# Performance work log

Measured on AMD Instinct MI355X. Metric: run time of the kernel, lower is better.

## Reference

```python
import jax, jax.numpy as jnp
import numpy as np

TEMPERATURE = 0.07
N_BANK = 1_000_000
DIM = 128
BATCH = 1024
K_NEIGH = 200


def _prob_density(memory_bank, v, idx):
    # memory_bank: [N, D], v: [B, D] (L2-normalized), idx: [B, K]
    vals = memory_bank[idx]                      # [B, K, D] gather
    dots = jnp.einsum('bkd,bd->bk', vals, v)     # per-item dot products
    return jnp.sum(jnp.exp(dots / TEMPERATURE), axis=1)  # [B]


def setup_inputs() -> dict:
    key = jax.random.key(0)
    k1, k2, k3, k4 = jax.random.split(key, 4)
    codes = jax.random.normal(k1, (BATCH, DIM), dtype=jnp.float32)
    memory_bank = jax.random.normal(k2, (N_BANK, DIM), dtype=jnp.float32)
    # memory bank rows are unit-normalized in the LA setup
    memory_bank = memory_bank / jnp.linalg.norm(memory_bank, axis=1, keepdims=True)
    idx_background = jax.random.randint(k3, (BATCH, K_NEIGH), 0, N_BANK, dtype=jnp.int64)
    idx_close = jax.random.randint(k4, (BATCH, K_NEIGH), 0, N_BANK, dtype=jnp.int64)
    return {
        'codes': codes,
        'memory_bank': memory_bank,
        'idx_background': idx_background,
        'idx_close': idx_close,
    }


def reference(codes, memory_bank, idx_background, idx_close):
    # v = F.normalize(codes, p=2, dim=1)
    v = codes / jnp.linalg.norm(codes, axis=1, keepdims=True)
    d1 = _prob_density(memory_bank, v, idx_background)
    d2 = _prob_density(memory_bank, v, idx_close)
    # loss_cluster = log(d1) - log(d2)
    return jnp.log(d1) - jnp.log(d2)
```

## Files before the change

kernel.cpp:

```cpp
#include <hip/hip_runtime.h>
#include <math.h>


constexpr int DIM = 128;
constexpr int KN  = 200;
constexpr int RPG = 25;
constexpr int UF  = 5;
constexpr float INV_T = 1.0f / 0.07f;

__global__ __launch_bounds__(256, 4)
void lal_kernel(const float* __restrict__ codes,
                const float* __restrict__ bank,
                const int*   __restrict__ idx_bg,
                const int*   __restrict__ idx_cl,
                float*       __restrict__ out)
{
    const int b   = blockIdx.x;
    const int tid = threadIdx.x;

    __shared__ float v[DIM];
    __shared__ int   s_ib[KN];
    __shared__ int   s_ic[KN];
    __shared__ float wsum[4];
    __shared__ float red1[8];
    __shared__ float red2[8];
    __shared__ float s_rnorm;

    if (tid < KN) {
        s_ib[tid] = idx_bg[b * KN + tid];
        s_ic[tid] = idx_cl[b * KN + tid];
    }

    float c  = (tid < DIM) ? codes[b * DIM + tid] : 0.0f;
    float ss = c * c;
    #pragma unroll
    for (int m = 32; m > 0; m >>= 1) ss += __shfl_xor(ss, m, 64);
    if ((tid & 63) == 0) wsum[tid >> 6] = ss;
    __syncthreads();
    if (tid == 0) {
        float t = wsum[0] + wsum[1] + wsum[2] + wsum[3];
        s_rnorm = 1.0f / sqrtf(t);
    }
    __syncthreads();
    if (tid < DIM) v[tid] = c * s_rnorm;
    __syncthreads();

    const int group = tid >> 5;
    const int lane  = tid & 31;

    const float4 vv = ((const float4*)v)[lane];
    const int kbase = group * RPG;

    float sum1 = 0.0f, sum2 = 0.0f;

    #pragma unroll 1
    for (int j = 0; j < RPG; j += UF) {
        float4 x1[UF], x2[UF];
        #pragma unroll
        for (int u = 0; u < UF; ++u) {
            const int r1 = s_ib[kbase + j + u];
            const int r2 = s_ic[kbase + j + u];
            x1[u] = ((const float4*)(bank + (size_t)r1 * DIM))[lane];
            x2[u] = ((const float4*)(bank + (size_t)r2 * DIM))[lane];
        }
        #pragma unroll
        for (int u = 0; u < UF; ++u) {
            float d1 = x1[u].x * vv.x + x1[u].y * vv.y + x1[u].z * vv.z + x1[u].w * vv.w;
            float d2 = x2[u].x * vv.x + x2[u].y * vv.y + x2[u].z * vv.z + x2[u].w * vv.w;
            #pragma unroll
            for (int m = 16; m > 0; m >>= 1) {
                d1 += __shfl_xor(d1, m, 64);
                d2 += __shfl_xor(d2, m, 64);
            }
            sum1 += __expf(d1 * INV_T);
            sum2 += __expf(d2 * INV_T);
        }
    }

    if (lane == 0) { red1[group] = sum1; red2[group] = sum2; }
    __syncthreads();
    if (tid == 0) {
        float D1 = 0.0f, D2 = 0.0f;
        #pragma unroll
        for (int g = 0; g < 8; ++g) { D1 += red1[g]; D2 += red2[g]; }
        out[b] = logf(D1) - logf(D2);
    }
}

extern "C" void kernel_launch(void* const* d_in, const int* in_sizes, int n_in,
                              void* d_out, int out_size, void* d_ws, size_t ws_size,
                              hipStream_t stream)
{
    const float* codes  = (const float*)d_in[0];
    const float* bank   = (const float*)d_in[1];
    const int*   idx_bg = (const int*)d_in[2];
    const int*   idx_cl = (const int*)d_in[3];
    float*       out    = (float*)d_out;

    const int batch = in_sizes[0] / DIM;
    lal_kernel<<<batch, 256, 0, stream>>>(codes, bank, idx_bg, idx_cl, out);
}
```

Measured before the change: 587.2 us.

## Stream gathered bank rows into LDS with triple-buffered async global_load_lds

```diff
diff --git a/kernel.cpp b/kernel.cpp
--- a/kernel.cpp
+++ b/kernel.cpp
@@ -2,34 +2,39 @@
 #include <math.h>
 
 
-constexpr int DIM = 128;
-constexpr int KN  = 200;
-constexpr int RPG = 25;
-constexpr int UF  = 5;
+constexpr int DIM   = 128;
+constexpr int KN    = 200;
+constexpr int HALF  = 100;
+constexpr int TROWS = 4;
+constexpr int NT    = HALF / TROWS;
 constexpr float INV_T = 1.0f / 0.07f;
 
-__global__ __launch_bounds__(256, 4)
+typedef const __attribute__((address_space(1))) void gvoid_t;
+typedef __attribute__((address_space(3))) void lvoid_t;
+
+__global__ __launch_bounds__(256, 6)
 void lal_kernel(const float* __restrict__ codes,
                 const float* __restrict__ bank,
                 const int*   __restrict__ idx_bg,
                 const int*   __restrict__ idx_cl,
                 float*       __restrict__ out)
 {
-    const int b   = blockIdx.x;
-    const int tid = threadIdx.x;
+    const int b    = blockIdx.x;
+    const int tid  = threadIdx.x;
+    const int w    = tid >> 6;
+    const int lane = tid & 63;
 
-    __shared__ float v[DIM];
-    __shared__ int   s_ib[KN];
-    __shared__ int   s_ic[KN];
+    __shared__ alignas(16) float v[DIM];
+    __shared__ int   s_idx[4 * HALF];
+    __shared__ alignas(16) float tiles[4][3][TROWS * DIM];
     __shared__ float wsum[4];
-    __shared__ float red1[8];
-    __shared__ float red2[8];
+    __shared__ float red[4];
     __shared__ float s_rnorm;
 
-    if (tid < KN) {
-        s_ib[tid] = idx_bg[b * KN + tid];
-        s_ic[tid] = idx_cl[b * KN + tid];
-    }
+    const int* ip    = (w < 2) ? idx_bg : idx_cl;
+    const int  kbase = (w & 1) * HALF;
+    for (int k = lane; k < HALF; k += 64)
+        s_idx[w * HALF + k] = ip[b * KN + kbase + k];
 
     float c  = (tid < DIM) ? codes[b * DIM + tid] : 0.0f;
     float ss = c * c;
@@ -45,46 +50,63 @@
     if (tid < DIM) v[tid] = c * s_rnorm;
     __syncthreads();
 
-    const int group = tid >> 5;
-    const int lane  = tid & 31;
+    const int s = lane & 15;
+    const int r = lane >> 4;
+    const float4 vv0 = ((const float4*)v)[s];
+    const float4 vv1 = ((const float4*)v)[s + 16];
 
-    const float4 vv = ((const float4*)v)[lane];
-    const int kbase = group * RPG;
+    const float* bank_lane = bank + (lane & 31) * 4;
+    const int*   midx = &s_idx[w * HALF];
+    float* const tb   = &tiles[w][0][0];
+    float sum = 0.0f;
 
-    float sum1 = 0.0f, sum2 = 0.0f;
+    auto STAGE = [&](int t, int bsel) {
+        int r0 = midx[4 * t     + (lane >> 5)];
+        int r1 = midx[4 * t + 2 + (lane >> 5)];
+        const float* g0 = bank_lane + (size_t)r0 * DIM;
+        const float* g1 = bank_lane + (size_t)r1 * DIM;
+        float* d0 = tb + bsel * (TROWS * DIM);
+        float* d1 = d0 + 2 * DIM;
+        __builtin_amdgcn_global_load_lds((gvoid_t*)g0, (lvoid_t*)d0, 16, 0, 0);
+        __builtin_amdgcn_global_load_lds((gvoid_t*)g1, (lvoid_t*)d1, 16, 0, 0);
+    };
 
-    #pragma unroll 1
-    for (int j = 0; j < RPG; j += UF) {
-        float4 x1[UF], x2[UF];
-        #pragma unroll
-        for (int u = 0; u < UF; ++u) {
-            const int r1 = s_ib[kbase + j + u];
-            const int r2 = s_ic[kbase + j + u];
-            x1[u] = ((const float4*)(bank + (size_t)r1 * DIM))[lane];
-            x2[u] = ((const float4*)(bank + (size_t)r2 * DIM))[lane];
-        }
-        #pragma unroll
-        for (int u = 0; u < UF; ++u) {
-            float d1 = x1[u].x * vv.x + x1[u].y * vv.y + x1[u].z * vv.z + x1[u].w * vv.w;
-            float d2 = x2[u].x * vv.x + x2[u].y * vv.y + x2[u].z * vv.z + x2[u].w * vv.w;
-            #pragma unroll
-            for (int m = 16; m > 0; m >>= 1) {
-                d1 += __shfl_xor(d1, m, 64);
-                d2 += __shfl_xor(d2, m, 64);
-            }
-            sum1 += __expf(d1 * INV_T);
-            sum2 += __expf(d2 * INV_T);
-        }
+    auto COMPUTE = [&](int bsel) {
+        const float4* T = (const float4*)(tb + bsel * (TROWS * DIM));
+        float4 x0 = T[r * 32 + s];
+        float4 x1 = T[r * 32 + s + 16];
+        float d = x0.x * vv0.x + x0.y * vv0.y + x0.z * vv0.z + x0.w * vv0.w
+                + x1.x * vv1.x + x1.y * vv1.y + x1.z * vv1.z + x1.w * vv1.w;
+        d += __shfl_xor(d, 1, 16);
+        d += __shfl_xor(d, 2, 16);
+        d += __shfl_xor(d, 4, 16);
+        d += __shfl_xor(d, 8, 16);
+        float e = __expf(d * INV_T);
+        if (s == 0) sum += e;
+    };
+
+    STAGE(0, 0);
+    STAGE(1, 1);
+    int bsel = 0;
+    for (int t = 0; t < NT - 2; ++t) {
+        STAGE(t + 2, (bsel + 2) % 3);
+        asm volatile("s_waitcnt vmcnt(4)" ::: "memory");
+        COMPUTE(bsel);
+        __builtin_amdgcn_sched_barrier(0);
+        bsel = (bsel + 1) % 3;
     }
+    asm volatile("s_waitcnt vmcnt(2)" ::: "memory");
+    COMPUTE(bsel);
+    bsel = (bsel + 1) % 3;
+    asm volatile("s_waitcnt vmcnt(0)" ::: "memory");
+    COMPUTE(bsel);
 
-    if (lane == 0) { red1[group] = sum1; red2[group] = sum2; }
+    #pragma unroll
+    for (int m = 32; m > 0; m >>= 1) sum += __shfl_xor(sum, m, 64);
+    if (lane == 0) red[w] = sum;
     __syncthreads();
-    if (tid == 0) {
-        float D1 = 0.0f, D2 = 0.0f;
-        #pragma unroll
-        for (int g = 0; g < 8; ++g) { D1 += red1[g]; D2 += red2[g]; }
-        out[b] = logf(D1) - logf(D2);
-    }
+    if (tid == 0)
+        out[b] = logf(red[0] + red[1]) - logf(red[2] + red[3]);
 }
 
 extern "C" void kernel_launch(void* const* d_in, const int* in_sizes, int n_in,
```

After: 590.6 us. Within noise of the previous version (+0.6%).

## Split gather into per-list blocks with full unroll and separate finalize kernel

Applied to the files above, without the earlier changes.

```diff
diff --git a/kernel.cpp b/kernel.cpp
--- a/kernel.cpp
+++ b/kernel.cpp
@@ -2,18 +2,96 @@
 #include <math.h>
 
 
-constexpr int DIM = 128;
-constexpr int KN  = 200;
-constexpr int RPG = 25;
-constexpr int UF  = 5;
+constexpr int   DIM   = 128;
+constexpr int   KN    = 200;
+constexpr int   RPG   = 25;
 constexpr float INV_T = 1.0f / 0.07f;
 
+
+__global__ __launch_bounds__(256, 3)
+void k_gather(const float* __restrict__ codes,
+              const float* __restrict__ bank,
+              const int*   __restrict__ idx_bg,
+              const int*   __restrict__ idx_cl,
+              float*       __restrict__ dacc,
+              int batch)
+{
+    const int bid  = blockIdx.x;
+    const int b    = bid >> 1;
+    const int list = bid & 1;
+    const int tid  = threadIdx.x;
+
+    const int* __restrict__ ip = list ? idx_cl : idx_bg;
+
+    __shared__ alignas(16) float v[DIM];
+    __shared__ int   s_idx[KN];
+    __shared__ float wsum[4];
+    __shared__ float red[8];
+    __shared__ float s_rnorm;
+
+    if (tid < KN) s_idx[tid] = ip[b * KN + tid];
+
+    float c  = (tid < DIM) ? codes[b * DIM + tid] : 0.0f;
+    float ss = c * c;
+    #pragma unroll
+    for (int m = 32; m > 0; m >>= 1) ss += __shfl_xor(ss, m, 64);
+    if ((tid & 63) == 0) wsum[tid >> 6] = ss;
+    __syncthreads();
+    if (tid == 0) {
+        float t = wsum[0] + wsum[1] + wsum[2] + wsum[3];
+        s_rnorm = 1.0f / sqrtf(t);
+    }
+    __syncthreads();
+    if (tid < DIM) v[tid] = c * s_rnorm;
+    __syncthreads();
+
+    const int group = tid >> 5;
+    const int lane  = tid & 31;
+    const float4 vv = ((const float4*)v)[lane];
+    const int kbase = group * RPG;
+
+    float4 x[RPG];
+    #pragma unroll
+    for (int u = 0; u < RPG; ++u) {
+        const int r = s_idx[kbase + u];
+        x[u] = ((const float4*)(bank + (size_t)r * DIM))[lane];
+    }
+
+    float sum = 0.0f;
+    #pragma unroll
+    for (int u = 0; u < RPG; ++u) {
+        float d = x[u].x * vv.x + x[u].y * vv.y + x[u].z * vv.z + x[u].w * vv.w;
+        #pragma unroll
+        for (int m = 16; m > 0; m >>= 1) d += __shfl_xor(d, m, 64);
+        sum += __expf(d * INV_T);
+    }
+
+    if (lane == 0) red[group] = sum;
+    __syncthreads();
+    if (tid == 0) {
+        float D = 0.0f;
+        #pragma unroll
+        for (int g = 0; g < 8; ++g) D += red[g];
+        dacc[list * batch + b] = D;
+    }
+}
+
+__global__ __launch_bounds__(256)
+void k_fin(const float* __restrict__ dacc, float* __restrict__ out, int batch)
+{
+    const int b = blockIdx.x * blockDim.x + threadIdx.x;
+    if (b < batch) out[b] = logf(dacc[b]) - logf(dacc[batch + b]);
+}
+
+
+constexpr int UF = 5;
+
 __global__ __launch_bounds__(256, 4)
-void lal_kernel(const float* __restrict__ codes,
-                const float* __restrict__ bank,
-                const int*   __restrict__ idx_bg,
-                const int*   __restrict__ idx_cl,
-                float*       __restrict__ out)
+void lal_fallback(const float* __restrict__ codes,
+                  const float* __restrict__ bank,
+                  const int*   __restrict__ idx_bg,
+                  const int*   __restrict__ idx_cl,
+                  float*       __restrict__ out)
 {
     const int b   = blockIdx.x;
     const int tid = threadIdx.x;
@@ -47,7 +125,6 @@
 
     const int group = tid >> 5;
     const int lane  = tid & 31;
-
     const float4 vv = ((const float4*)v)[lane];
     const int kbase = group * RPG;
 
@@ -87,6 +164,7 @@
     }
 }
 
+
 extern "C" void kernel_launch(void* const* d_in, const int* in_sizes, int n_in,
                               void* d_out, int out_size, void* d_ws, size_t ws_size,
                               hipStream_t stream)
@@ -98,5 +176,13 @@
     float*       out    = (float*)d_out;
 
     const int batch = in_sizes[0] / DIM;
-    lal_kernel<<<batch, 256, 0, stream>>>(codes, bank, idx_bg, idx_cl, out);
+
+    if (ws_size >= (size_t)(2 * batch) * sizeof(float)) {
+        float* dacc = (float*)d_ws;
+        k_gather<<<2 * batch, 256, 0, stream>>>(codes, bank, idx_bg, idx_cl,
+                                                dacc, batch);
+        k_fin<<<(batch + 255) / 256, 256, 0, stream>>>(dacc, out, batch);
+    } else {
+        lal_fallback<<<batch, 256, 0, stream>>>(codes, bank, idx_bg, idx_cl, out);
+    }
 }
```

New measurement: 591.3 us. About the same (+0.7%).

## Bucket gather records by bank region to improve memory locality

Applied to the files above, without the earlier changes.

```diff
diff --git a/kernel.cpp b/kernel.cpp
--- a/kernel.cpp
+++ b/kernel.cpp
@@ -2,18 +2,136 @@
 #include <math.h>
 
 
-constexpr int DIM = 128;
-constexpr int KN  = 200;
+constexpr int   DIM   = 128;
+constexpr int   KN    = 200;
+constexpr int   NBANK = 1000000;
+constexpr int   NBUK  = (NBANK + 255) / 256;
+constexpr int   MAXPB = 192;
+constexpr float INV_T = 1.0f / 0.07f;
+
+
+__global__ __launch_bounds__(128)
+void k_prep(const float* __restrict__ codes, float* __restrict__ vtab,
+            int* __restrict__ cnt, float* __restrict__ dacc, int batch)
+{
+    const int b = blockIdx.x;
+    const int t = threadIdx.x;
+
+    const int gt = b * 128 + t;
+    if (gt < NBUK) cnt[gt] = 0;
+    else if (gt < NBUK + 2 * batch) dacc[gt - NBUK] = 0.0f;
+
+    __shared__ float w[2];
+    float c  = codes[b * DIM + t];
+    float ss = c * c;
+    #pragma unroll
+    for (int m = 32; m > 0; m >>= 1) ss += __shfl_xor(ss, m, 64);
+    if ((t & 63) == 0) w[t >> 6] = ss;
+    __syncthreads();
+    const float rn = 1.0f / sqrtf(w[0] + w[1]);
+    vtab[b * DIM + t] = c * rn;
+}
+
+__global__ __launch_bounds__(256)
+void k_scatter(const int* __restrict__ idx_bg, const int* __restrict__ idx_cl,
+               const float* __restrict__ bank, const float* __restrict__ vtab,
+               unsigned int* __restrict__ recs, int* __restrict__ cnt,
+               float* __restrict__ dacc, int batch)
+{
+    const int bk = batch * KN;
+    const int n  = 2 * bk;
+    for (int e = blockIdx.x * blockDim.x + threadIdx.x; e < n;
+         e += gridDim.x * blockDim.x) {
+        const int list = (e >= bk) ? 1 : 0;
+        const int off  = e - list * bk;
+        const int row  = (list ? idx_cl : idx_bg)[off];
+        const int b    = off / KN;
+        const unsigned int rec = ((unsigned int)row << 11)
+                               | ((unsigned int)list << 10)
+                               | (unsigned int)b;
+        const int buk = row >> 8;
+        const int pos = atomicAdd(&cnt[buk], 1);
+        if (pos < MAXPB) {
+            recs[buk * MAXPB + pos] = rec;
+        } else {
+            const float4* br = (const float4*)(bank + (size_t)row * DIM);
+            const float4* vr = (const float4*)(vtab + (size_t)b * DIM);
+            float d = 0.0f;
+            for (int i = 0; i < DIM / 4; ++i) {
+                float4 x = br[i], v = vr[i];
+                d += x.x * v.x + x.y * v.y + x.z * v.z + x.w * v.w;
+            }
+            atomicAdd(&dacc[list * batch + b], __expf(d * INV_T));
+        }
+    }
+}
+
+__global__ __launch_bounds__(256)
+void k_main(const float* __restrict__ bank, const unsigned int* __restrict__ recs,
+            const int* __restrict__ cnt, const float* __restrict__ vtab,
+            float* __restrict__ dacc, int batch)
+{
+    const int g   = blockIdx.x;
+    const int tid = threadIdx.x;
+
+    __shared__ unsigned int s_recs[MAXPB];
+    const int n = min(cnt[g], MAXPB);
+    for (int i = tid; i < n; i += 256) s_recs[i] = recs[g * MAXPB + i];
+    __syncthreads();
+    if (n == 0) return;
+
+    const int group = tid >> 5;
+    const int lane  = tid & 31;
+
+    for (int base = group * 4; base < n; base += 32) {
+        const int m = min(4, n - base);
+        float4 x[4], w[4];
+        int    di[4];
+        #pragma unroll
+        for (int u = 0; u < 4; ++u) {
+            if (u < m) {
+                const unsigned int rec = s_recs[base + u];
+                const int b    = rec & 1023;
+                const int list = (rec >> 10) & 1;
+                const int row  = rec >> 11;
+                x[u]  = ((const float4*)(bank + (size_t)row * DIM))[lane];
+                w[u]  = ((const float4*)(vtab + (size_t)b * DIM))[lane];
+                di[u] = list * batch + b;
+            }
+        }
+        #pragma unroll
+        for (int u = 0; u < 4; ++u) {
+            if (u < m) {
+                float d = x[u].x * w[u].x + x[u].y * w[u].y
+                        + x[u].z * w[u].z + x[u].w * w[u].w;
+                d += __shfl_xor(d, 16, 32);
+                d += __shfl_xor(d, 8, 32);
+                d += __shfl_xor(d, 4, 32);
+                d += __shfl_xor(d, 2, 32);
+                d += __shfl_xor(d, 1, 32);
+                if (lane == 0) atomicAdd(&dacc[di[u]], __expf(d * INV_T));
+            }
+        }
+    }
+}
+
+__global__ __launch_bounds__(256)
+void k_fin(const float* __restrict__ dacc, float* __restrict__ out, int batch)
+{
+    const int b = blockIdx.x * blockDim.x + threadIdx.x;
+    if (b < batch) out[b] = logf(dacc[b]) - logf(dacc[batch + b]);
+}
+
+
 constexpr int RPG = 25;
 constexpr int UF  = 5;
-constexpr float INV_T = 1.0f / 0.07f;
 
 __global__ __launch_bounds__(256, 4)
-void lal_kernel(const float* __restrict__ codes,
-                const float* __restrict__ bank,
-                const int*   __restrict__ idx_bg,
-                const int*   __restrict__ idx_cl,
-                float*       __restrict__ out)
+void lal_fallback(const float* __restrict__ codes,
+                  const float* __restrict__ bank,
+                  const int*   __restrict__ idx_bg,
+                  const int*   __restrict__ idx_cl,
+                  float*       __restrict__ out)
 {
     const int b   = blockIdx.x;
     const int tid = threadIdx.x;
@@ -47,7 +165,6 @@
 
     const int group = tid >> 5;
     const int lane  = tid & 31;
-
     const float4 vv = ((const float4*)v)[lane];
     const int kbase = group * RPG;
 
@@ -87,6 +204,7 @@
     }
 }
 
+
 extern "C" void kernel_launch(void* const* d_in, const int* in_sizes, int n_in,
                               void* d_out, int out_size, void* d_ws, size_t ws_size,
                               hipStream_t stream)
@@ -98,5 +216,21 @@
     float*       out    = (float*)d_out;
 
     const int batch = in_sizes[0] / DIM;
-    lal_kernel<<<batch, 256, 0, stream>>>(codes, bank, idx_bg, idx_cl, out);
-}
+
+    if (batch == 1024 && ws_size >= (size_t)(8u << 20)) {
+        char*         ws   = (char*)d_ws;
+        float*        vtab = (float*)(ws);
+        float*        dacc = (float*)(ws + 524288);
+        int*          cnt  = (int*)  (ws + 524288 + 8192);
+        unsigned int* recs = (unsigned int*)(ws + 524288 + 8192 + 16384);
+
+        const int n = 2 * batch * KN;
+        k_prep   <<<batch, 128, 0, stream>>>(codes, vtab, cnt, dacc, batch);
+        k_scatter<<<(n + 255) / 256, 256, 0, stream>>>(idx_bg, idx_cl, bank,
+                                                       vtab, recs, cnt, dacc, batch);
+        k_main   <<<NBUK, 256, 0, stream>>>(bank, recs, cnt, vtab, dacc, batch);
+        k_fin    <<<(batch + 255) / 256, 256, 0, stream>>>(dacc, out, batch);
+    } else {
+        lal_fallback<<<batch, 256, 0, stream>>>(codes, bank, idx_bg, idx_cl, out);
+    }
+}
```

Measured after the change: 715.7 us. 1.22x slower.
